# Performance work log

Hardware: AMD Instinct MI355X
Metric: run time of the kernel (lower is better)

## Reference

```python
import jax, jax.numpy as jnp
import numpy as np


def setup_inputs() -> dict:
    key = jax.random.key(0)
    k1, k2, k3, k4 = jax.random.split(key, 4)
    B, L, F, V = 512, 512, 64, 20000
    src_ids = jax.random.randint(k1, (B, L), 0, V, dtype=jnp.int32)
    dst_ids = jax.random.randint(k2, (B, L), 0, V, dtype=jnp.int32)
    # MLP params: Linear(1->F), ReLU, Linear(F->F)
    W1 = jax.random.normal(k3, (1, F), dtype=jnp.float32)  # fan_in = 1
    b1 = jnp.zeros((F,), dtype=jnp.float32)
    W2 = jax.random.normal(k4, (F, F), dtype=jnp.float32) * (1.0 / np.sqrt(F))
    b2 = jnp.zeros((F,), dtype=jnp.float32)
    return {"src_ids": src_ids, "dst_ids": dst_ids, "W1": W1, "b1": b1,
            "W2": W2, "b2": b2, "num_nodes": V}


def reference(src_ids, dst_ids, W1, b1, W2, b2, num_nodes):
    # Per-row histogram over node ids (vectorized replacement for
    # np.unique + dict gather in the torch code).
    row_hist = lambda r: jnp.bincount(r, length=num_nodes)
    hist_src = jax.vmap(row_hist)(src_ids)  # [B, V]
    hist_dst = jax.vmap(row_hist)(dst_ids)  # [B, V]

    gather = lambda h, ids: jnp.take_along_axis(h, ids, axis=1)  # [B, L]

    # appearances: [count in own seq, count in other seq], shape [B, L, 2]
    src_app = jnp.stack([gather(hist_src, src_ids), gather(hist_dst, src_ids)], axis=-1).astype(jnp.float32)
    dst_app = jnp.stack([gather(hist_src, dst_ids), gather(hist_dst, dst_ids)], axis=-1).astype(jnp.float32)
    # id 0 is padding -> zero both count channels
    src_app = jnp.where((src_ids == 0)[..., None], 0.0, src_app)
    dst_app = jnp.where((dst_ids == 0)[..., None], 0.0, dst_app)

    def encode(app):
        # app: [B, L, 2]; per-scalar MLP then sum over the 2 count channels
        h = jax.nn.relu(app[..., None] * W1[0] + b1)  # [B, L, 2, F]
        out = h @ W2 + b2                              # [B, L, 2, F]
        return out.sum(axis=2)                         # [B, L, F]

    return encode(src_app), encode(dst_app)
```

## Files before the change

kernel.cpp:

```cpp
#include <hip/hip_runtime.h>

constexpr int Bn = 512;
constexpr int Ln = 512;
constexpr int Fn = 64;
constexpr int Vn = 20000;
constexpr int HWORDS = (Vn + 2) / 3;
constexpr int BL = Bn * Ln;

typedef float f32x4 __attribute__((ext_vector_type(4)));

__global__ void build_table_kernel(const float* __restrict__ W1,
                                   const float* __restrict__ b1,
                                   const float* __restrict__ W2,
                                   const float* __restrict__ b2,
                                   float* __restrict__ table) {
    const int v = blockIdx.x;
    const int j = threadIdx.x;
    __shared__ float h[Fn];
    h[j] = fmaxf((float)v * W1[j] + b1[j], 0.0f);
    __syncthreads();
    float acc = b2[j];
#pragma unroll
    for (int i = 0; i < Fn; ++i)
        acc = fmaf(h[i], W2[i * Fn + j], acc);
    table[v * Fn + j] = acc;
}

__device__ __forceinline__ unsigned hist_get(const unsigned* __restrict__ h, int v) {
    const int w = v / 3;
    const int f = v - w * 3;
    return (h[w] >> (10 * f)) & 0x3FFu;
}

__global__ __launch_bounds__(512) void fused_kernel(
    const int* __restrict__ src_ids,
    const int* __restrict__ dst_ids,
    const float* __restrict__ table,
    float* __restrict__ out) {
    __shared__ unsigned hs[HWORDS];
    __shared__ unsigned hd[HWORDS];
    __shared__ unsigned pc[2 * Ln];

    const int b = blockIdx.x;
    const int tid = threadIdx.x;

    for (int i = tid; i < HWORDS; i += 512) { hs[i] = 0u; hd[i] = 0u; }
    __syncthreads();

    const int s = src_ids[b * Ln + tid];
    const int d = dst_ids[b * Ln + tid];
    {
        int w;
        w = s / 3; atomicAdd(&hs[w], 1u << (10 * (s - w * 3)));
        w = d / 3; atomicAdd(&hd[w], 1u << (10 * (d - w * 3)));
    }
    __syncthreads();

    {
        unsigned ws = 0u, wd = 0u;
        if (s != 0) ws = hist_get(hs, s) | (hist_get(hd, s) << 16);
        if (d != 0) wd = hist_get(hs, d) | (hist_get(hd, d) << 16);
        pc[tid] = ws;
        pc[Ln + tid] = wd;
    }
    __syncthreads();

    const f32x4* __restrict__ t4 = (const f32x4*)table;
    f32x4* __restrict__ out4 = (f32x4*)out;
    const size_t row0 = (size_t)b * Ln;
#pragma unroll 4
    for (int it = 0; it < 32; ++it) {
        const unsigned g = (unsigned)it * 512u + tid;
        const unsigned r = g & 15u;
        const unsigned idx = g >> 4;
        const unsigned a = idx >> 9;
        const unsigned l = idx & 511u;
        const unsigned wrd = pc[idx];
        const unsigned c0 = wrd & 0xFFFFu;
        const unsigned c1 = wrd >> 16;
        const f32x4 t0 = t4[c0 * 16u + r];
        const f32x4 t1 = t4[c1 * 16u + r];
        const f32x4 o = t0 + t1;
        __builtin_nontemporal_store(o, &out4[((size_t)a * BL + row0 + l) * 16u + r]);
    }
}

extern "C" void kernel_launch(void* const* d_in, const int* in_sizes, int n_in,
                              void* d_out, int out_size, void* d_ws, size_t ws_size,
                              hipStream_t stream) {
    const int*   src_ids = (const int*)d_in[0];
    const int*   dst_ids = (const int*)d_in[1];
    const float* W1      = (const float*)d_in[2];
    const float* b1      = (const float*)d_in[3];
    const float* W2      = (const float*)d_in[4];
    const float* b2      = (const float*)d_in[5];

    float* table = (float*)d_ws;

    build_table_kernel<<<Ln + 1, Fn, 0, stream>>>(W1, b1, W2, b2, table);
    fused_kernel<<<Bn, 512, 0, stream>>>(src_ids, dst_ids, table, (float*)d_out);
}
```

Measured before the change: 154.8 us.

## Fuse MLP table build into main kernel with small shared-memory table

```diff
diff --git a/kernel.cpp b/kernel.cpp
--- a/kernel.cpp
+++ b/kernel.cpp
@@ -6,25 +6,9 @@
 constexpr int Vn = 20000;
 constexpr int HWORDS = (Vn + 2) / 3;
 constexpr int BL = Bn * Ln;
+constexpr int TROWS = 16;
 
 typedef float f32x4 __attribute__((ext_vector_type(4)));
-
-__global__ void build_table_kernel(const float* __restrict__ W1,
-                                   const float* __restrict__ b1,
-                                   const float* __restrict__ W2,
-                                   const float* __restrict__ b2,
-                                   float* __restrict__ table) {
-    const int v = blockIdx.x;
-    const int j = threadIdx.x;
-    __shared__ float h[Fn];
-    h[j] = fmaxf((float)v * W1[j] + b1[j], 0.0f);
-    __syncthreads();
-    float acc = b2[j];
-#pragma unroll
-    for (int i = 0; i < Fn; ++i)
-        acc = fmaf(h[i], W2[i * Fn + j], acc);
-    table[v * Fn + j] = acc;
-}
 
 __device__ __forceinline__ unsigned hist_get(const unsigned* __restrict__ h, int v) {
     const int w = v / 3;
@@ -32,23 +16,60 @@
     return (h[w] >> (10 * f)) & 0x3FFu;
 }
 
+__device__ __noinline__ f32x4 table_row4(float v, unsigned r,
+                                         const float* __restrict__ W1,
+                                         const float* __restrict__ b1,
+                                         const float* __restrict__ W2,
+                                         const float* __restrict__ b2) {
+    const int j0 = (int)r * 4;
+    f32x4 acc = { b2[j0], b2[j0 + 1], b2[j0 + 2], b2[j0 + 3] };
+    for (int i = 0; i < Fn; ++i) {
+        const float h = fmaxf(fmaf(v, W1[i], b1[i]), 0.0f);
+        acc.x = fmaf(h, W2[i * Fn + j0 + 0], acc.x);
+        acc.y = fmaf(h, W2[i * Fn + j0 + 1], acc.y);
+        acc.z = fmaf(h, W2[i * Fn + j0 + 2], acc.z);
+        acc.w = fmaf(h, W2[i * Fn + j0 + 3], acc.w);
+    }
+    return acc;
+}
+
 __global__ __launch_bounds__(512) void fused_kernel(
     const int* __restrict__ src_ids,
     const int* __restrict__ dst_ids,
-    const float* __restrict__ table,
+    const float* __restrict__ W1,
+    const float* __restrict__ b1,
+    const float* __restrict__ W2,
+    const float* __restrict__ b2,
     float* __restrict__ out) {
     __shared__ unsigned hs[HWORDS];
     __shared__ unsigned hd[HWORDS];
     __shared__ unsigned pc[2 * Ln];
+    __shared__ float tl[TROWS][Fn];
 
     const int b = blockIdx.x;
     const int tid = threadIdx.x;
 
     for (int i = tid; i < HWORDS; i += 512) { hs[i] = 0u; hd[i] = 0u; }
-    __syncthreads();
 
     const int s = src_ids[b * Ln + tid];
     const int d = dst_ids[b * Ln + tid];
+
+    {
+        const int j = tid & 63;
+#pragma unroll
+        for (int k = 0; k < 2; ++k) {
+            const int v = (tid >> 6) + 8 * k;
+            float acc = b2[j];
+#pragma unroll
+            for (int i = 0; i < Fn; ++i) {
+                const float h = fmaxf(fmaf((float)v, W1[i], b1[i]), 0.0f);
+                acc = fmaf(h, W2[i * Fn + j], acc);
+            }
+            tl[v][j] = acc;
+        }
+    }
+    __syncthreads();
+
     {
         int w;
         w = s / 3; atomicAdd(&hs[w], 1u << (10 * (s - w * 3)));
@@ -65,23 +86,25 @@
     }
     __syncthreads();
 
-    const f32x4* __restrict__ t4 = (const f32x4*)table;
+    const f32x4* __restrict__ tl4 = (const f32x4*)&tl[0][0];
     f32x4* __restrict__ out4 = (f32x4*)out;
-    const size_t row0 = (size_t)b * Ln;
+    const unsigned row16 = (unsigned)b * (Ln * 16u);
 #pragma unroll 4
     for (int it = 0; it < 32; ++it) {
         const unsigned g = (unsigned)it * 512u + tid;
         const unsigned r = g & 15u;
         const unsigned idx = g >> 4;
         const unsigned a = idx >> 9;
-        const unsigned l = idx & 511u;
-        const unsigned wrd = pc[idx];
-        const unsigned c0 = wrd & 0xFFFFu;
-        const unsigned c1 = wrd >> 16;
-        const f32x4 t0 = t4[c0 * 16u + r];
-        const f32x4 t1 = t4[c1 * 16u + r];
+        const unsigned w = pc[idx];
+        const unsigned c0 = w & 0xFFFFu;
+        const unsigned c1 = w >> 16;
+        f32x4 t0, t1;
+        if (c0 < (unsigned)TROWS) t0 = tl4[c0 * 16u + r];
+        else                      t0 = table_row4((float)c0, r, W1, b1, W2, b2);
+        if (c1 < (unsigned)TROWS) t1 = tl4[c1 * 16u + r];
+        else                      t1 = table_row4((float)c1, r, W1, b1, W2, b2);
         const f32x4 o = t0 + t1;
-        __builtin_nontemporal_store(o, &out4[((size_t)a * BL + row0 + l) * 16u + r]);
+        out4[a * (BL * 16u) + row16 + (g & 8191u)] = o;
     }
 }
 
@@ -95,8 +118,6 @@
     const float* W2      = (const float*)d_in[4];
     const float* b2      = (const float*)d_in[5];
 
-    float* table = (float*)d_ws;
-
-    build_table_kernel<<<Ln + 1, Fn, 0, stream>>>(W1, b1, W2, b2, table);
-    fused_kernel<<<Bn, 512, 0, stream>>>(src_ids, dst_ids, table, (float*)d_out);
+    fused_kernel<<<Bn, 512, 0, stream>>>(src_ids, dst_ids, W1, b1, W2, b2,
+                                         (float*)d_out);
 }
```

Measured after the change: 149.6 us. 3.4% less time.
